# Kernel optimization log

Hardware: AMD Instinct MI355X
Metric: run time of the kernel (lower is better)

## Reference

```python
import jax, jax.numpy as jnp
import numpy as np

NUM_HEADS = 4
DIM_MODEL = 256
DIM_HEAD = DIM_MODEL // NUM_HEADS  # 64


def _conv1x1(w, b, x):
    # Conv1d kernel_size=1: [B, D_in, N] -> [B, D_out, N]
    return jnp.einsum('oi,bin->bon', w, x) + b[None, :, None]


def setup_inputs() -> dict:
    key = jax.random.key(0)
    ks = jax.random.split(key, 12)
    B, D, N = 8, DIM_MODEL, 2048
    s = 1.0 / np.sqrt(D)
    inp = {
        'query': jax.random.normal(ks[0], (B, D, N), dtype=jnp.float32),
        'key': jax.random.normal(ks[1], (B, D, N), dtype=jnp.float32),
        'value': jax.random.normal(ks[2], (B, D, N), dtype=jnp.float32),
        'wq': jax.random.normal(ks[3], (D, D), dtype=jnp.float32) * s,
        'bq': jax.random.normal(ks[4], (D,), dtype=jnp.float32) * 0.01,
        'wk': jax.random.normal(ks[5], (D, D), dtype=jnp.float32) * s,
        'bk': jax.random.normal(ks[6], (D,), dtype=jnp.float32) * 0.01,
        'wv': jax.random.normal(ks[7], (D, D), dtype=jnp.float32) * s,
        'bv': jax.random.normal(ks[8], (D,), dtype=jnp.float32) * 0.01,
        'wm': jax.random.normal(ks[9], (D, D), dtype=jnp.float32) * s,
        'bm': jax.random.normal(ks[10], (D,), dtype=jnp.float32) * 0.01,
    }
    return inp


def reference(query, key, value, wq, bq, wk, bk, wv, bv, wm, bm):
    B = query.shape[0]
    d, h = DIM_HEAD, NUM_HEADS
    # 1x1 conv projections, then split channels as (dim_head, num_heads) per torch view
    q = _conv1x1(wq, bq, query).reshape(B, d, h, -1)  # [B, d, h, N]
    k = _conv1x1(wk, bk, key).reshape(B, d, h, -1)    # [B, d, h, M]
    v = _conv1x1(wv, bv, value).reshape(B, d, h, -1)  # [B, d, h, M]
    norm = 1.0 / float(d) ** 0.5
    scores = jnp.einsum('bdhn,bdhm->bhnm', q, k) * norm  # [B, h, N, M]
    prob = jax.nn.softmax(scores, axis=-1)
    attn = jnp.einsum('bhnm,bdhm->bdhn', prob, v)        # [B, d, h, N]
    out = _conv1x1(wm, bm, attn.reshape(B, d * h, -1))   # [B, D, N]
    return out
```

## Files before the change

kernel.cpp:

```cpp
#include <hip/hip_runtime.h>
#include <math.h>

#define BB 8
#define DD 256
#define NN 2048
#define NH 4
#define DH 64

typedef _Float16 half8   __attribute__((ext_vector_type(8)));
typedef _Float16 half4_t __attribute__((ext_vector_type(4)));
typedef _Float16 half2_t __attribute__((ext_vector_type(2)));
typedef float    floatx4 __attribute__((ext_vector_type(4)));

#define MFMA32(A, B, C) __builtin_amdgcn_mfma_f32_16x16x32_f16(A, B, C, 0, 0, 0)

#define SC 0.18033688011112042f

__global__ __launch_bounds__(256) void prep_weights(
    const float* __restrict__ wq, const float* __restrict__ wk,
    const float* __restrict__ wv, const float* __restrict__ wm,
    _Float16* __restrict__ wqf, _Float16* __restrict__ wkf,
    _Float16* __restrict__ wvf, _Float16* __restrict__ wmf)
{
    int id = blockIdx.x * 256 + threadIdx.x;
    wqf[id] = (_Float16)wq[id];
    wkf[id] = (_Float16)wk[id];
    wvf[id] = (_Float16)wv[id];
    int row = id >> 8, col = id & 255;
    int hh = col >> 6, dd = col & 63;
    wmf[id] = (_Float16)wm[row * 256 + dd * 4 + hh];
}

__global__ __launch_bounds__(256, 3) void conv_qkv(
    const _Float16* __restrict__ wqf, const _Float16* __restrict__ wkf,
    const _Float16* __restrict__ wvf,
    const float* __restrict__ bq, const float* __restrict__ bk,
    const float* __restrict__ bv,
    const float* __restrict__ Xq, const float* __restrict__ Xk,
    const float* __restrict__ Xv,
    _Float16* __restrict__ Yq, _Float16* __restrict__ Yk,
    _Float16* __restrict__ Yv)
{
    const int n0 = blockIdx.x * 64;
    const int b  = blockIdx.y;
    const int z  = blockIdx.z;
    const _Float16* Wf = z == 0 ? wqf : (z == 1 ? wkf : wvf);
    const float* bias  = z == 0 ? bq  : (z == 1 ? bk  : bv);
    const float* X     = z == 0 ? Xq  : (z == 1 ? Xk  : Xv);
    const float osc    = z == 0 ? SC : 1.0f;

    const int t = threadIdx.x;
    const int w = t >> 6, l = t & 63, c = l & 15, q = l >> 4;

    __shared__ _Float16 smem[64 * 264 + 9216];
    _Float16* Xs = smem;
    _Float16* Es = smem + 64 * 264;

    const int gk = (c & 3) << 1;

    {
        const int nb = t & 15, kb = t >> 4;
        const int slot = (kb >> 1), sub = (kb & 1) * 4;
        #pragma unroll
        for (int cc = 0; cc < 4; ++cc) {
            const float* Xg = X + (size_t)b * DD * NN +
                              (size_t)(cc * 64 + kb * 4) * NN + n0 + nb * 4;
            float4 x[4];
            #pragma unroll
            for (int i = 0; i < 4; ++i) x[i] = *(const float4*)(Xg + (size_t)i * NN);
            #pragma unroll
            for (int j = 0; j < 4; ++j) {
                half4_t hv;
                #pragma unroll
                for (int i = 0; i < 4; ++i) hv[i] = (_Float16)(((const float*)&x[i])[j]);
                *(half4_t*)(Xs + (nb * 4 + j) * 264 +
                            (((cc * 8 + slot) ^ (j << 1)) << 3) + sub) = hv;
            }
        }
    }
    __syncthreads();

    for (int hf = 0; hf < 2; ++hf) {
        const int cout0 = hf * 128;

        half8 af[2][8];
        {
            const _Float16* wp = Wf + (size_t)(cout0 + w * 32 + c) * 256 + q * 8;
            #pragma unroll
            for (int rt = 0; rt < 2; ++rt)
                #pragma unroll
                for (int ch = 0; ch < 8; ++ch)
                    af[rt][ch] = *(const half8*)(wp + rt * 16 * 256 + ch * 32);
        }

        floatx4 acc[2][4];
        #pragma unroll
        for (int rt = 0; rt < 2; ++rt)
            #pragma unroll
            for (int nt = 0; nt < 4; ++nt) acc[rt][nt] = (floatx4){0.f, 0.f, 0.f, 0.f};

        #pragma unroll
        for (int ch = 0; ch < 8; ++ch)
            #pragma unroll
            for (int nt = 0; nt < 4; ++nt) {
                half8 bx = *(const half8*)(Xs + (nt * 16 + c) * 264 +
                                           (((ch * 4 + q) ^ gk) << 3));
                acc[0][nt] = MFMA32(af[0][ch], bx, acc[0][nt]);
                acc[1][nt] = MFMA32(af[1][ch], bx, acc[1][nt]);
            }

        if (z < 2) {
            __syncthreads();
            #pragma unroll
            for (int rt = 0; rt < 2; ++rt)
                #pragma unroll
                for (int nt = 0; nt < 4; ++nt) {
                    half4_t hv;
                    #pragma unroll
                    for (int r = 0; r < 4; ++r)
                        hv[r] = (_Float16)((acc[rt][nt][r] +
                                bias[cout0 + w * 32 + rt * 16 + q * 4 + r]) * osc);
                    *(half4_t*)(Es + (nt * 16 + c) * 136 + w * 32 + rt * 16 + q * 4) = hv;
                }
            __syncthreads();
            _Float16* Y = z == 0 ? Yq : Yk;
            const int nn = t >> 2, hh = t & 3;
            half8 hv[4];
            #pragma unroll
            for (int i = 0; i < 4; ++i)
                #pragma unroll
                for (int k = 0; k < 8; ++k)
                    hv[i][k] = Es[nn * 136 + (i * 8 + k) * 4 + hh];
            _Float16* dst = Y + ((size_t)(b * NH + hh) * NN + n0 + nn) * 64 + hf * 32;
            #pragma unroll
            for (int i = 0; i < 4; ++i) *(half8*)(dst + i * 8) = hv[i];
        } else {
            __syncthreads();
            #pragma unroll
            for (int rt = 0; rt < 2; ++rt)
                #pragma unroll
                for (int nt = 0; nt < 4; ++nt)
                    #pragma unroll
                    for (int r = 0; r < 4; ++r)
                        Es[(w * 32 + rt * 16 + q * 4 + r) * 72 + nt * 16 + c] =
                            (_Float16)(acc[rt][nt][r] +
                                       bias[cout0 + w * 32 + rt * 16 + q * 4 + r]);
            __syncthreads();
            const int cl = t >> 1, noff = (t & 1) * 32;
            const int cout = cout0 + cl;
            const int hh = cout & 3, dd = cout >> 2;
            _Float16* dst = Yv + ((size_t)(b * NH + hh) * 64 + dd) * NN + n0 + noff;
            #pragma unroll
            for (int i = 0; i < 4; ++i)
                *(half8*)(dst + i * 8) = *(const half8*)(Es + cl * 72 + noff + i * 8);
        }
    }
}

__global__ __launch_bounds__(256, 3) void conv_o(
    const _Float16* __restrict__ Wf, const float* __restrict__ bias,
    const _Float16* __restrict__ At, float* __restrict__ out)
{
    const int n0 = blockIdx.x * 64;
    const int b  = blockIdx.y;
    const int hf = blockIdx.z;
    const int cout0 = hf * 128;

    const int t = threadIdx.x;
    const int w = t >> 6, l = t & 63, c = l & 15, q = l >> 4;

    __shared__ float fs[128 * 66];

    half8 af[2][8];
    {
        const _Float16* wp = Wf + (size_t)(cout0 + w * 32 + c) * 256 + q * 8;
        #pragma unroll
        for (int rt = 0; rt < 2; ++rt)
            #pragma unroll
            for (int ch = 0; ch < 8; ++ch)
                af[rt][ch] = *(const half8*)(wp + rt * 16 * 256 + ch * 32);
    }

    floatx4 acc[2][4];
    #pragma unroll
    for (int rt = 0; rt < 2; ++rt)
        #pragma unroll
        for (int nt = 0; nt < 4; ++nt) acc[rt][nt] = (floatx4){0.f, 0.f, 0.f, 0.f};

    #pragma unroll
    for (int ch = 0; ch < 8; ++ch)
        #pragma unroll
        for (int nt = 0; nt < 4; ++nt) {
            half8 bx = *(const half8*)(At +
                ((size_t)b * NN + n0 + nt * 16 + c) * 256 + ch * 32 + q * 8);
            acc[0][nt] = MFMA32(af[0][ch], bx, acc[0][nt]);
            acc[1][nt] = MFMA32(af[1][ch], bx, acc[1][nt]);
        }

    #pragma unroll
    for (int rt = 0; rt < 2; ++rt)
        #pragma unroll
        for (int nt = 0; nt < 4; ++nt)
            #pragma unroll
            for (int r = 0; r < 4; ++r)
                fs[(w * 32 + rt * 16 + q * 4 + r) * 66 + nt * 16 + c] =
                    acc[rt][nt][r] + bias[cout0 + w * 32 + rt * 16 + q * 4 + r];
    __syncthreads();
    const int cl = t >> 1, noff = (t & 1) * 32;
    float* dst = out + (size_t)b * DD * NN + (size_t)(cout0 + cl) * NN + n0 + noff;
    #pragma unroll
    for (int i = 0; i < 8; ++i)
        *(float4*)(dst + i * 4) = *(const float4*)(fs + cl * 66 + noff + i * 4);
}

__global__ __launch_bounds__(512) void attn_mfma6(
    const _Float16* __restrict__ Qt, const _Float16* __restrict__ Kt,
    const _Float16* __restrict__ V, _Float16* __restrict__ At)
{
    const int n0 = blockIdx.x * 128;
    const int h  = blockIdx.y;
    const int b  = blockIdx.z;
    const int t  = threadIdx.x;
    const int w  = t >> 6, l = t & 63, c = l & 15, q = l >> 4;

    const size_t bh = (size_t)(b * NH + h);

    __shared__ _Float16 smem[2 * 17920];

    half8 bq2[2];
    #pragma unroll
    for (int ch = 0; ch < 2; ++ch)
        bq2[ch] = *(const half8*)(Qt + (bh * NN + n0 + w * 16 + c) * 64 + ch * 32 + q * 8);

    float lp = 0.f;
    floatx4 o[4];
    #pragma unroll
    for (int dt = 0; dt < 4; ++dt) o[dt] = (floatx4){0.f, 0.f, 0.f, 0.f};

    const int ksr = t >> 2, ksc = (t & 3) * 16;
    const int vr  = t >> 3, vcb = (t & 7) * 16;
    const _Float16* Kg = Kt + bh * NN * 64;
    const _Float16* Vg = V + bh * 64 * NN;

    const int gk  = (c & 3) << 1;
    const int rk0 = ((0 + q) ^ gk) << 3;
    const int rk1 = ((4 + q) ^ gk) << 3;
    int rv[4];
    #pragma unroll
    for (int mt2 = 0; mt2 < 4; ++mt2) rv[mt2] = ((mt2 * 4 + q) ^ gk) << 3;
    const int gK  = (ksr & 3) << 1;
    const int s0  = (t & 3) * 2;
    const int wk0 = (s0 ^ gK) << 3;
    const int wk1 = ((s0 + 1) ^ gK) << 3;
    const int gV  = (vr & 3) << 1;

    half8 kpre[2], vpre[2];
    kpre[0] = *(const half8*)(Kg + (size_t)ksr * 64 + ksc);
    kpre[1] = *(const half8*)(Kg + (size_t)ksr * 64 + ksc + 8);
    vpre[0] = *(const half8*)(Vg + (size_t)vr * NN + vcb);
    vpre[1] = *(const half8*)(Vg + (size_t)vr * NN + vcb + 8);

#define STAGE_TILE(KSP, VSP)                                                    \
    {                                                                           \
        *(half8*)((KSP) + ksr * 72 + wk0) = kpre[0];                            \
        *(half8*)((KSP) + ksr * 72 + wk1) = kpre[1];                            \
        _Pragma("unroll")                                                       \
        for (int u = 0; u < 2; ++u) {                                           \
            const int mb = vcb + u * 8;                                         \
            const int p0 = (mb & ~31) + (((mb >> 2) & 3) << 3) +                \
                           (((mb >> 4) & 1) << 2);                              \
            const int sl = p0 >> 3, sub = p0 & 7;                               \
            half4_t lo, hi;                                                     \
            _Pragma("unroll")                                                   \
            for (int j = 0; j < 4; ++j) { lo[j] = vpre[u][j]; hi[j] = vpre[u][4 + j]; } \
            *(half4_t*)((VSP) + vr * 136 + ((sl ^ gV) << 3) + sub)       = lo;  \
            *(half4_t*)((VSP) + vr * 136 + (((sl + 1) ^ gV) << 3) + sub) = hi;  \
        }                                                                       \
    }

    STAGE_TILE(smem, smem + 9216);
    kpre[0] = *(const half8*)(Kg + (size_t)(128 + ksr) * 64 + ksc);
    kpre[1] = *(const half8*)(Kg + (size_t)(128 + ksr) * 64 + ksc + 8);
    vpre[0] = *(const half8*)(Vg + (size_t)vr * NN + 128 + vcb);
    vpre[1] = *(const half8*)(Vg + (size_t)vr * NN + 128 + vcb + 8);
    __syncthreads();

    for (int it = 0; it < 16; ++it) {
        if (it < 15) {
            _Float16* Ksw = smem + ((it + 1) & 1) * 17920;
            _Float16* Vsw = Ksw + 9216;
            STAGE_TILE(Ksw, Vsw);
        }
        {
            const int mn = (it + 2 < 16) ? (it + 2) * 128 : it * 128;
            kpre[0] = *(const half8*)(Kg + (size_t)(mn + ksr) * 64 + ksc);
            kpre[1] = *(const half8*)(Kg + (size_t)(mn + ksr) * 64 + ksc + 8);
            vpre[0] = *(const half8*)(Vg + (size_t)vr * NN + mn + vcb);
            vpre[1] = *(const half8*)(Vg + (size_t)vr * NN + mn + vcb + 8);
        }
        const _Float16* Ks = smem + (it & 1) * 17920;
        const _Float16* Vs = Ks + 9216;
        #pragma unroll
        for (int mt2 = 0; mt2 < 4; ++mt2) {
            half8 p8;
            #pragma unroll
            for (int hfm = 0; hfm < 2; ++hfm) {
                const int mt = mt2 * 2 + hfm;
                floatx4 s = {0.f, 0.f, 0.f, 0.f};
                half8 ak0 = *(const half8*)(Ks + (mt * 16 + c) * 72 + rk0);
                s = MFMA32(ak0, bq2[0], s);
                half8 ak1 = *(const half8*)(Ks + (mt * 16 + c) * 72 + rk1);
                s = MFMA32(ak1, bq2[1], s);
                float e0 = exp2f(s[0]), e1 = exp2f(s[1]);
                float e2 = exp2f(s[2]), e3 = exp2f(s[3]);
                lp += (e0 + e1) + (e2 + e3);
                half2_t c01 = __builtin_bit_cast(half2_t, __builtin_amdgcn_cvt_pkrtz(e0, e1));
                half2_t c23 = __builtin_bit_cast(half2_t, __builtin_amdgcn_cvt_pkrtz(e2, e3));
                p8[hfm * 4 + 0] = c01[0]; p8[hfm * 4 + 1] = c01[1];
                p8[hfm * 4 + 2] = c23[0]; p8[hfm * 4 + 3] = c23[1];
            }
            #pragma unroll
            for (int dt = 0; dt < 4; ++dt) {
                half8 av = *(const half8*)(Vs + (dt * 16 + c) * 136 + rv[mt2]);
                o[dt] = MFMA32(av, p8, o[dt]);
            }
        }
        __syncthreads();
    }
#undef STAGE_TILE

    lp += __shfl_xor(lp, 16);
    lp += __shfl_xor(lp, 32);
    const float inv = 1.f / lp;

    _Float16* fsm = smem;
    #pragma unroll
    for (int dt = 0; dt < 4; ++dt) {
        half4_t hv;
        #pragma unroll
        for (int r = 0; r < 4; ++r) hv[r] = (_Float16)(o[dt][r] * inv);
        *(half4_t*)(fsm + (w * 16 + c) * 72 + dt * 16 + q * 4) = hv;
    }
    __syncthreads();
    const int rn = t >> 2, seg = (t & 3) * 16;
    _Float16* dst = At + ((size_t)b * NN + n0 + rn) * 256 + h * 64 + seg;
    *(half8*)(dst)     = *(const half8*)(fsm + rn * 72 + seg);
    *(half8*)(dst + 8) = *(const half8*)(fsm + rn * 72 + seg + 8);
}

extern "C" void kernel_launch(void* const* d_in, const int* in_sizes, int n_in,
                              void* d_out, int out_size, void* d_ws, size_t ws_size,
                              hipStream_t stream) {
    const float* query = (const float*)d_in[0];
    const float* key_  = (const float*)d_in[1];
    const float* value = (const float*)d_in[2];
    const float* wq    = (const float*)d_in[3];
    const float* bq    = (const float*)d_in[4];
    const float* wk    = (const float*)d_in[5];
    const float* bk    = (const float*)d_in[6];
    const float* wv    = (const float*)d_in[7];
    const float* bv    = (const float*)d_in[8];
    const float* wm    = (const float*)d_in[9];
    const float* bm    = (const float*)d_in[10];
    float* out = (float*)d_out;

    _Float16* ws = (_Float16*)d_ws;
    _Float16* wqf = ws;
    _Float16* wkf = wqf + 65536;
    _Float16* wvf = wkf + 65536;
    _Float16* wmf = wvf + 65536;
    const size_t e16 = (size_t)BB * NH * NN * DH;
    _Float16* qf = ws + 262144;
    _Float16* kf = qf + e16;
    _Float16* vf = kf + e16;
    _Float16* at = vf + e16;

    prep_weights<<<256, 256, 0, stream>>>(wq, wk, wv, wm, wqf, wkf, wvf, wmf);
    conv_qkv<<<dim3(32, 8, 3), 256, 0, stream>>>(wqf, wkf, wvf, bq, bk, bv,
                                                 query, key_, value, qf, kf, vf);
    attn_mfma6<<<dim3(16, 4, 8), 512, 0, stream>>>(qf, kf, vf, at);
    conv_o<<<dim3(32, 8, 2), 256, 0, stream>>>(wmf, bm, at, out);
}
```

Measured before the change: 202.0 us.

## Give each attention wave two query tiles to reuse K/V fragments

The attention kernel now runs 256 threads per block, and each wave processes two 16-row query tiles, so every K and V fragment loaded from shared memory feeds two MFMAs. Global-to-shared staging is widened to four 16-byte vectors per thread. The XOR swizzle on the shared K/V layouts is removed, which simplifies addressing but may add LDS bank conflicts. Register use per thread roughly doubles for accumulators, and there are fewer waves per block to hide latency.

```diff
diff --git a/kernel.cpp b/kernel.cpp
--- a/kernel.cpp
+++ b/kernel.cpp
@@ -213,7 +213,7 @@
         *(float4*)(dst + i * 4) = *(const float4*)(fs + cl * 66 + noff + i * 4);
 }
 
-__global__ __launch_bounds__(512) void attn_mfma6(
+__global__ __launch_bounds__(256, 2) void attn_mfma7(
     const _Float16* __restrict__ Qt, const _Float16* __restrict__ Kt,
     const _Float16* __restrict__ V, _Float16* __restrict__ At)
 {
@@ -227,125 +227,132 @@
 
     __shared__ _Float16 smem[2 * 17920];
 
-    half8 bq2[2];
-    #pragma unroll
-    for (int ch = 0; ch < 2; ++ch)
-        bq2[ch] = *(const half8*)(Qt + (bh * NN + n0 + w * 16 + c) * 64 + ch * 32 + q * 8);
-
-    float lp = 0.f;
-    floatx4 o[4];
-    #pragma unroll
-    for (int dt = 0; dt < 4; ++dt) o[dt] = (floatx4){0.f, 0.f, 0.f, 0.f};
-
-    const int ksr = t >> 2, ksc = (t & 3) * 16;
-    const int vr  = t >> 3, vcb = (t & 7) * 16;
+    half8 bq2[2][2];
+    #pragma unroll
+    for (int jj = 0; jj < 2; ++jj)
+        #pragma unroll
+        for (int ch = 0; ch < 2; ++ch)
+            bq2[jj][ch] = *(const half8*)(Qt +
+                (bh * NN + n0 + w * 32 + jj * 16 + c) * 64 + ch * 32 + q * 8);
+
+    float lp0 = 0.f, lp1 = 0.f;
+    floatx4 o[2][4];
+    #pragma unroll
+    for (int jj = 0; jj < 2; ++jj)
+        #pragma unroll
+        for (int dt = 0; dt < 4; ++dt) o[jj][dt] = (floatx4){0.f, 0.f, 0.f, 0.f};
+
+    const int ksr = t >> 1, ksc = (t & 1) * 32;
+    const int vr  = t >> 2, vcb = (t & 3) * 32;
     const _Float16* Kg = Kt + bh * NN * 64;
     const _Float16* Vg = V + bh * 64 * NN;
 
-    const int gk  = (c & 3) << 1;
-    const int rk0 = ((0 + q) ^ gk) << 3;
-    const int rk1 = ((4 + q) ^ gk) << 3;
-    int rv[4];
-    #pragma unroll
-    for (int mt2 = 0; mt2 < 4; ++mt2) rv[mt2] = ((mt2 * 4 + q) ^ gk) << 3;
-    const int gK  = (ksr & 3) << 1;
-    const int s0  = (t & 3) * 2;
-    const int wk0 = (s0 ^ gK) << 3;
-    const int wk1 = ((s0 + 1) ^ gK) << 3;
-    const int gV  = (vr & 3) << 1;
-
-    half8 kpre[2], vpre[2];
-    kpre[0] = *(const half8*)(Kg + (size_t)ksr * 64 + ksc);
-    kpre[1] = *(const half8*)(Kg + (size_t)ksr * 64 + ksc + 8);
-    vpre[0] = *(const half8*)(Vg + (size_t)vr * NN + vcb);
-    vpre[1] = *(const half8*)(Vg + (size_t)vr * NN + vcb + 8);
+    half8 kpre[4], vpre[4];
+    #pragma unroll
+    for (int u = 0; u < 4; ++u) {
+        kpre[u] = *(const half8*)(Kg + (size_t)ksr * 64 + ksc + u * 8);
+        vpre[u] = *(const half8*)(Vg + (size_t)vr * NN + vcb + u * 8);
+    }
 
 #define STAGE_TILE(KSP, VSP)                                                    \
     {                                                                           \
-        *(half8*)((KSP) + ksr * 72 + wk0) = kpre[0];                            \
-        *(half8*)((KSP) + ksr * 72 + wk1) = kpre[1];                            \
         _Pragma("unroll")                                                       \
-        for (int u = 0; u < 2; ++u) {                                           \
+        for (int u = 0; u < 4; ++u)                                             \
+            *(half8*)((KSP) + ksr * 72 + ksc + u * 8) = kpre[u];                \
+        _Pragma("unroll")                                                       \
+        for (int u = 0; u < 4; ++u) {                                           \
             const int mb = vcb + u * 8;                                         \
             const int p0 = (mb & ~31) + (((mb >> 2) & 3) << 3) +                \
                            (((mb >> 4) & 1) << 2);                              \
-            const int sl = p0 >> 3, sub = p0 & 7;                               \
             half4_t lo, hi;                                                     \
             _Pragma("unroll")                                                   \
             for (int j = 0; j < 4; ++j) { lo[j] = vpre[u][j]; hi[j] = vpre[u][4 + j]; } \
-            *(half4_t*)((VSP) + vr * 136 + ((sl ^ gV) << 3) + sub)       = lo;  \
-            *(half4_t*)((VSP) + vr * 136 + (((sl + 1) ^ gV) << 3) + sub) = hi;  \
+            *(half4_t*)((VSP) + vr * 136 + p0)     = lo;                        \
+            *(half4_t*)((VSP) + vr * 136 + p0 + 8) = hi;                        \
         }                                                                       \
     }
 
     STAGE_TILE(smem, smem + 9216);
-    kpre[0] = *(const half8*)(Kg + (size_t)(128 + ksr) * 64 + ksc);
-    kpre[1] = *(const half8*)(Kg + (size_t)(128 + ksr) * 64 + ksc + 8);
-    vpre[0] = *(const half8*)(Vg + (size_t)vr * NN + 128 + vcb);
-    vpre[1] = *(const half8*)(Vg + (size_t)vr * NN + 128 + vcb + 8);
+    #pragma unroll
+    for (int u = 0; u < 4; ++u) {
+        kpre[u] = *(const half8*)(Kg + (size_t)(128 + ksr) * 64 + ksc + u * 8);
+        vpre[u] = *(const half8*)(Vg + (size_t)vr * NN + 128 + vcb + u * 8);
+    }
     __syncthreads();
 
     for (int it = 0; it < 16; ++it) {
         if (it < 15) {
             _Float16* Ksw = smem + ((it + 1) & 1) * 17920;
-            _Float16* Vsw = Ksw + 9216;
-            STAGE_TILE(Ksw, Vsw);
+            STAGE_TILE(Ksw, Ksw + 9216);
         }
         {
             const int mn = (it + 2 < 16) ? (it + 2) * 128 : it * 128;
-            kpre[0] = *(const half8*)(Kg + (size_t)(mn + ksr) * 64 + ksc);
-            kpre[1] = *(const half8*)(Kg + (size_t)(mn + ksr) * 64 + ksc + 8);
-            vpre[0] = *(const half8*)(Vg + (size_t)vr * NN + mn + vcb);
-            vpre[1] = *(const half8*)(Vg + (size_t)vr * NN + mn + vcb + 8);
+            #pragma unroll
+            for (int u = 0; u < 4; ++u) {
+                kpre[u] = *(const half8*)(Kg + (size_t)(mn + ksr) * 64 + ksc + u * 8);
+                vpre[u] = *(const half8*)(Vg + (size_t)vr * NN + mn + vcb + u * 8);
+            }
         }
         const _Float16* Ks = smem + (it & 1) * 17920;
         const _Float16* Vs = Ks + 9216;
         #pragma unroll
         for (int mt2 = 0; mt2 < 4; ++mt2) {
-            half8 p8;
+            half8 p8[2];
             #pragma unroll
             for (int hfm = 0; hfm < 2; ++hfm) {
                 const int mt = mt2 * 2 + hfm;
-                floatx4 s = {0.f, 0.f, 0.f, 0.f};
-                half8 ak0 = *(const half8*)(Ks + (mt * 16 + c) * 72 + rk0);
-                s = MFMA32(ak0, bq2[0], s);
-                half8 ak1 = *(const half8*)(Ks + (mt * 16 + c) * 72 + rk1);
-                s = MFMA32(ak1, bq2[1], s);
-                float e0 = exp2f(s[0]), e1 = exp2f(s[1]);
-                float e2 = exp2f(s[2]), e3 = exp2f(s[3]);
-                lp += (e0 + e1) + (e2 + e3);
-                half2_t c01 = __builtin_bit_cast(half2_t, __builtin_amdgcn_cvt_pkrtz(e0, e1));
-                half2_t c23 = __builtin_bit_cast(half2_t, __builtin_amdgcn_cvt_pkrtz(e2, e3));
-                p8[hfm * 4 + 0] = c01[0]; p8[hfm * 4 + 1] = c01[1];
-                p8[hfm * 4 + 2] = c23[0]; p8[hfm * 4 + 3] = c23[1];
+                half8 ak0 = *(const half8*)(Ks + (mt * 16 + c) * 72 + q * 8);
+                half8 ak1 = *(const half8*)(Ks + (mt * 16 + c) * 72 + 32 + q * 8);
+                #pragma unroll
+                for (int jj = 0; jj < 2; ++jj) {
+                    floatx4 s = {0.f, 0.f, 0.f, 0.f};
+                    s = MFMA32(ak0, bq2[jj][0], s);
+                    s = MFMA32(ak1, bq2[jj][1], s);
+                    float e0 = exp2f(s[0]), e1 = exp2f(s[1]);
+                    float e2 = exp2f(s[2]), e3 = exp2f(s[3]);
+                    if (jj == 0) lp0 += (e0 + e1) + (e2 + e3);
+                    else         lp1 += (e0 + e1) + (e2 + e3);
+                    half2_t c01 = __builtin_bit_cast(half2_t, __builtin_amdgcn_cvt_pkrtz(e0, e1));
+                    half2_t c23 = __builtin_bit_cast(half2_t, __builtin_amdgcn_cvt_pkrtz(e2, e3));
+                    p8[jj][hfm * 4 + 0] = c01[0]; p8[jj][hfm * 4 + 1] = c01[1];
+                    p8[jj][hfm * 4 + 2] = c23[0]; p8[jj][hfm * 4 + 3] = c23[1];
+                }
             }
             #pragma unroll
             for (int dt = 0; dt < 4; ++dt) {
-                half8 av = *(const half8*)(Vs + (dt * 16 + c) * 136 + rv[mt2]);
-                o[dt] = MFMA32(av, p8, o[dt]);
+                half8 av = *(const half8*)(Vs + (dt * 16 + c) * 136 + mt2 * 32 + q * 8);
+                o[0][dt] = MFMA32(av, p8[0], o[0][dt]);
+                o[1][dt] = MFMA32(av, p8[1], o[1][dt]);
             }
         }
         __syncthreads();
     }
 #undef STAGE_TILE
 
-    lp += __shfl_xor(lp, 16);
-    lp += __shfl_xor(lp, 32);
-    const float inv = 1.f / lp;
+    lp0 += __shfl_xor(lp0, 16); lp0 += __shfl_xor(lp0, 32);
+    lp1 += __shfl_xor(lp1, 16); lp1 += __shfl_xor(lp1, 32);
+    const float inv0 = 1.f / lp0, inv1 = 1.f / lp1;
 
     _Float16* fsm = smem;
     #pragma unroll
-    for (int dt = 0; dt < 4; ++dt) {
-        half4_t hv;
-        #pragma unroll
-        for (int r = 0; r < 4; ++r) hv[r] = (_Float16)(o[dt][r] * inv);
-        *(half4_t*)(fsm + (w * 16 + c) * 72 + dt * 16 + q * 4) = hv;
+    for (int jj = 0; jj < 2; ++jj) {
+        const float inv = jj == 0 ? inv0 : inv1;
+        #pragma unroll
+        for (int dt = 0; dt < 4; ++dt) {
+            half4_t hv;
+            #pragma unroll
+            for (int r = 0; r < 4; ++r) hv[r] = (_Float16)(o[jj][dt][r] * inv);
+            *(half4_t*)(fsm + (w * 32 + jj * 16 + c) * 72 + dt * 16 + q * 4) = hv;
+        }
     }
     __syncthreads();
-    const int rn = t >> 2, seg = (t & 3) * 16;
-    _Float16* dst = At + ((size_t)b * NN + n0 + rn) * 256 + h * 64 + seg;
-    *(half8*)(dst)     = *(const half8*)(fsm + rn * 72 + seg);
-    *(half8*)(dst + 8) = *(const half8*)(fsm + rn * 72 + seg + 8);
+    #pragma unroll
+    for (int rr = 0; rr < 2; ++rr) {
+        const int rn = rr * 64 + (t >> 2), seg = (t & 3) * 16;
+        _Float16* dst = At + ((size_t)b * NN + n0 + rn) * 256 + h * 64 + seg;
+        *(half8*)(dst)     = *(const half8*)(fsm + rn * 72 + seg);
+        *(half8*)(dst + 8) = *(const half8*)(fsm + rn * 72 + seg + 8);
+    }
 }
 
 extern "C" void kernel_launch(void* const* d_in, const int* in_sizes, int n_in,
@@ -378,6 +385,6 @@
     prep_weights<<<256, 256, 0, stream>>>(wq, wk, wv, wm, wqf, wkf, wvf, wmf);
     conv_qkv<<<dim3(32, 8, 3), 256, 0, stream>>>(wqf, wkf, wvf, bq, bk, bv,
                                                  query, key_, value, qf, kf, vf);
-    attn_mfma6<<<dim3(16, 4, 8), 512, 0, stream>>>(qf, kf, vf, at);
+    attn_mfma7<<<dim3(16, 4, 8), 256, 0, stream>>>(qf, kf, vf, at);
     conv_o<<<dim3(32, 8, 2), 256, 0, stream>>>(wmf, bm, at, out);
 }
```

Result: no change. 202.1 us (+0.0%).
